# Performance work log

Hardware: AMD Instinct MI355X
Metric: run time of the kernel (lower is better)

## Reference

```python
import jax, jax.numpy as jnp
import numpy as np

B, H, W = 8, 256, 256
NF = 64          # num_feat
E = 12           # num_expert
D = NF * 4       # token dim = 256
CD = D * E       # expanded dim = 3072


def _lrelu(x):
    return jnp.where(x >= 0, x, 0.2 * x)


def _conv(x, w, stride, pad):
    return jax.lax.conv_general_dilated(
        x, w, (stride, stride), [(pad, pad), (pad, pad)],
        dimension_numbers=('NCHW', 'OIHW', 'NCHW'))


def _bn(x, g, b):
    # training-mode BatchNorm2d: batch statistics over (N, H, W)
    m = jnp.mean(x, axis=(0, 2, 3), keepdims=True)
    v = jnp.var(x, axis=(0, 2, 3), keepdims=True)
    xn = (x - m) * jax.lax.rsqrt(v + 1e-5)
    return xn * g[None, :, None, None] + b[None, :, None, None]


def setup_inputs() -> dict:
    key = jax.random.key(0)
    ks = jax.random.split(key, 16)
    s = 0.05
    d = {}
    d['x'] = jax.random.normal(ks[0], (B, 3, H, W), jnp.float32)
    d['conv0_w'] = jax.random.normal(ks[1], (NF, 3, 3, 3)) * s
    d['conv0_b'] = jnp.zeros((NF,))
    d['conv1_w'] = jax.random.normal(ks[2], (NF, NF, 4, 4)) * s
    d['bn1_g'] = jnp.ones((NF,)); d['bn1_b'] = jnp.zeros((NF,))
    d['conv2_w'] = jax.random.normal(ks[3], (2 * NF, NF, 3, 3)) * s
    d['bn2_g'] = jnp.ones((2 * NF,)); d['bn2_b'] = jnp.zeros((2 * NF,))
    d['conv3_w'] = jax.random.normal(ks[4], (2 * NF, 2 * NF, 4, 4)) * s
    d['bn3_g'] = jnp.ones((2 * NF,)); d['bn3_b'] = jnp.zeros((2 * NF,))
    d['conv4_w'] = jax.random.normal(ks[5], (4 * NF, 2 * NF, 3, 3)) * s
    d['bn4_g'] = jnp.ones((4 * NF,)); d['bn4_b'] = jnp.zeros((4 * NF,))
    d['conv5_w'] = jax.random.normal(ks[6], (4 * NF, 4 * NF, 3, 3)) * s
    d['bn5_g'] = jnp.ones((4 * NF,)); d['bn5_b'] = jnp.zeros((4 * NF,))
    d['conv6_w'] = jax.random.normal(ks[7], (4 * NF, 4 * NF, 3, 3)) * s
    d['bn6_g'] = jnp.ones((4 * NF,)); d['bn6_b'] = jnp.zeros((4 * NF,))
    d['w_gating'] = jax.random.normal(ks[8], (D, E))          # torch.randn init
    d['body_w'] = jax.random.normal(ks[9], (D, CD)) * s       # Linear(c_dim, c_dim*blocks)
    d['body_b'] = jnp.zeros((CD,))
    d['ortho_w'] = jax.random.normal(ks[10], (1, 1, CD))      # OrthorTransform weight
    d['cls_w1'] = jax.random.normal(ks[11], (D, NF // 2)) * s # shared classifier
    d['cls_b1'] = jnp.zeros((NF // 2,))
    d['cls_w2'] = jax.random.normal(ks[12], (NF // 2, 1)) * s
    d['cls_b2'] = jnp.zeros((1,))
    return d


def reference(x, conv0_w, conv0_b, conv1_w, bn1_g, bn1_b, conv2_w, bn2_g, bn2_b,
              conv3_w, bn3_g, bn3_b, conv4_w, bn4_g, bn4_b, conv5_w, bn5_g, bn5_b,
              conv6_w, bn6_g, bn6_b, w_gating, body_w, body_b, ortho_w,
              cls_w1, cls_b1, cls_w2, cls_b2):
    # --- FE conv stack ---
    h = _lrelu(_conv(x, conv0_w, 1, 1) + conv0_b[None, :, None, None])
    h = _lrelu(_bn(_conv(h, conv1_w, 2, 1), bn1_g, bn1_b))
    h = _lrelu(_bn(_conv(h, conv2_w, 1, 1), bn2_g, bn2_b))
    h = _lrelu(_bn(_conv(h, conv3_w, 2, 1), bn3_g, bn3_b))
    h = _lrelu(_bn(_conv(h, conv4_w, 1, 1), bn4_g, bn4_b))
    h = _lrelu(_bn(_conv(h, conv5_w, 1, 1), bn5_g, bn5_b))
    h = _lrelu(_bn(_conv(h, conv6_w, 1, 1), bn6_g, bn6_b))
    b, c, hh, ww = h.shape
    tok = h.reshape(b, c, hh * ww).transpose(0, 2, 1)            # (B, N, D)
    # --- softmax router ---
    routing = jax.nn.softmax(jnp.einsum('bnd,de->bne', tok, w_gating), axis=-1)
    # --- CodeReduction: Linear + lrelu, OrthorTransform multiply, lrelu ---
    feat = _lrelu(tok @ body_w + body_b)                         # (B, N, E*D)
    feat = _lrelu(feat * ortho_w)
    feat = feat.reshape(b, hh * ww, E, D)                        # torch.split chunks
    # --- shared expert MLP on every chunk (all classifiers alias one module) ---
    hid = _lrelu(jnp.einsum('bned,df->bnef', feat, cls_w1) + cls_b1)
    outs = (jnp.einsum('bnef,fo->bneo', hid, cls_w2) + cls_b2)[..., 0]  # (B,N,E)
    # --- top-1 select (equivalent to the torch.where cascade) ---
    idx = jnp.argmax(routing, axis=-1, keepdims=True)
    output = jnp.take_along_axis(outs, idx, axis=-1)             # (B, N, 1)
    return output
```

## Files before the change

kernel.cpp:

```cpp
#include <hip/hip_runtime.h>

__device__ __forceinline__ float lrelu(float x) { return x >= 0.f ? x : 0.2f * x; }

typedef const __attribute__((address_space(1))) void* gas_ptr;
typedef __attribute__((address_space(3))) void* las_ptr;

__global__ __launch_bounds__(256) void conv0_k(const float* __restrict__ x,
                                               const float* __restrict__ w,
                                               const float* __restrict__ bias,
                                               float* __restrict__ out) {
    __shared__ float sIn[3][34][34];
    __shared__ float sW[27][16];
    const int H = 256;
    int tid = threadIdx.x, tx = tid & 31, ty = tid >> 5;
    int tX = (blockIdx.x & 7) * 32, tY = (blockIdx.x >> 3) * 32;
    int b = blockIdx.y, cog = blockIdx.z * 16;
    float acc[4][16] = {};
    const float* inB = x + (size_t)b * 3 * H * H;
    for (int idx = tid; idx < 3 * 1156; idx += 256) {
        int ci = idx / 1156, r = idx % 1156, iy = r / 34, ix = r % 34;
        int gy = tY - 1 + iy, gx = tX - 1 + ix;
        float v = 0.f;
        if ((unsigned)gy < 256u && (unsigned)gx < 256u)
            v = inB[(ci * H + gy) * H + gx];
        sIn[ci][iy][ix] = v;
    }
    for (int idx = tid; idx < 27 * 16; idx += 256) {
        int co = idx & 15, rest = idx >> 4;
        sW[rest][co] = w[(cog + co) * 27 + rest];
    }
    __syncthreads();
#pragma unroll
    for (int ci = 0; ci < 3; ci++)
#pragma unroll
        for (int dy = 0; dy < 3; dy++)
#pragma unroll
            for (int dx = 0; dx < 3; dx++) {
                float a0 = sIn[ci][ty + dy][tx + dx];
                float a1 = sIn[ci][ty + 8 + dy][tx + dx];
                float a2 = sIn[ci][ty + 16 + dy][tx + dx];
                float a3 = sIn[ci][ty + 24 + dy][tx + dx];
                const float* wp = sW[ci * 9 + dy * 3 + dx];
#pragma unroll
                for (int co = 0; co < 16; co++) {
                    float wv = wp[co];
                    acc[0][co] += a0 * wv; acc[1][co] += a1 * wv;
                    acc[2][co] += a2 * wv; acc[3][co] += a3 * wv;
                }
            }
    float* outB = out + (size_t)(b * 64 + cog) * 67080;
#pragma unroll
    for (int co = 0; co < 16; co++) {
        float bv = bias[cog + co];
#pragma unroll
        for (int r = 0; r < 4; r++)
            outB[(size_t)co * 67080 + (size_t)(tY + ty + 8 * r + 1) * 260 +
                 tX + tx + 1] = lrelu(acc[r][co] + bv);
    }
}

template <int COG>
__global__ __launch_bounds__(256) void c4x4p_k(const float* __restrict__ in,
                                               const float* __restrict__ w,
                                               float* __restrict__ out,
                                               int Cin, int Cout, int Hin,
                                               int Hp, int Wp,
                                               int oHp, int oWp, int oOff) {
    __shared__ float sIn[2][4488];
    __shared__ float sW[2][16 * COG];
    const int Hout = Hin >> 1;
    const int tid = threadIdx.x, tx = tid & 31, ty = tid >> 5;
    const int tpr = Hout >> 5;
    const int tX = (blockIdx.x % tpr) * 32, tY = (blockIdx.x / tpr) * 32;
    const int b = blockIdx.y, cog = blockIdx.z * COG;
    const int HWin = Hp * Wp;
    const float* inB = in + (size_t)b * Cin * HWin;
    const int wvbase = tid & ~63;

    int gOff[5]; int lOff[5]; bool act[5];
#pragma unroll
    for (int r = 0; r < 5; r++) {
        int idx = tid + r * 256;
        bool a = idx < 1122;
        int row = idx / 17, c4 = idx % 17;
        gOff[r] = a ? ((2 * tY + row) * Wp + 2 * tX + 4 * c4) : 0;
        lOff[r] = (r * 256 + wvbase) * 4;
        act[r] = a;
    }
    const int wco = tid % COG, wt = tid / COG;
    const int wgo = ((cog + wco) * Cin) * 16 + wt;
    const bool wact = tid < 16 * COG;

    float acc[4][COG];
#pragma unroll
    for (int j = 0; j < 4; j++)
#pragma unroll
        for (int c = 0; c < COG; c++) acc[j][c] = 0.f;

#pragma unroll
    for (int r = 0; r < 5; r++)
        if (act[r])
            __builtin_amdgcn_global_load_lds((gas_ptr)(inB + gOff[r]),
                                             (las_ptr)(&sIn[0][lOff[r]]), 16, 0, 0);
    if (wact)
        __builtin_amdgcn_global_load_lds((gas_ptr)(w + wgo),
                                         (las_ptr)(&sW[0][wvbase]), 4, 0, 0);
    __syncthreads();

    for (int k = 0; k < Cin; k++) {
        const int cur = k & 1, nb = cur ^ 1;
        const bool more = (k + 1) < Cin;
        if (more) {
            const float* p = inB + (size_t)(k + 1) * HWin;
#pragma unroll
            for (int r = 0; r < 5; r++)
                if (act[r])
                    __builtin_amdgcn_global_load_lds(
                        (gas_ptr)(p + gOff[r]),
                        (las_ptr)(&sIn[nb][lOff[r]]), 16, 0, 0);
            if (wact)
                __builtin_amdgcn_global_load_lds(
                    (gas_ptr)(w + wgo + (k + 1) * 16),
                    (las_ptr)(&sW[nb][wvbase]), 4, 0, 0);
        }
        const float* sI = sIn[cur];
        const float* sw = sW[cur];
#pragma unroll
        for (int dy = 0; dy < 4; dy++)
#pragma unroll
            for (int dx = 0; dx < 4; dx++) {
                const float* bp = sI + (2 * ty + dy) * 68 + 2 * tx + dx;
                float a0 = bp[0];
                float a1 = bp[16 * 68];
                float a2 = bp[32 * 68];
                float a3 = bp[48 * 68];
                const float* wp = sw + (dy * 4 + dx) * COG;
#pragma unroll
                for (int c = 0; c < COG; c++) {
                    float wv = wp[c];
                    acc[0][c] += a0 * wv; acc[1][c] += a1 * wv;
                    acc[2][c] += a2 * wv; acc[3][c] += a3 * wv;
                }
            }
        __syncthreads();
    }

    float* outB = out + (size_t)(b * Cout + cog) * oHp * oWp;
#pragma unroll
    for (int c = 0; c < COG; c++)
#pragma unroll
        for (int r = 0; r < 4; r++)
            outB[(size_t)c * oHp * oWp +
                 (size_t)(tY + ty + 8 * r + oOff) * oWp + tX + tx + oOff] =
                acc[r][c];
}

template <int COG, bool PADDED>
__global__ __launch_bounds__(256) void c3x3_k(const float* __restrict__ in,
                                              const float* __restrict__ w,
                                              const float2* __restrict__ ss,
                                              float* __restrict__ out,
                                              int Cin, int Cout, int H,
                                              int Hp, int Wp,
                                              int oHp, int oWp, int oOff) {
    constexpr int RS = PADDED ? 36 : 34;
    constexpr int CI = 34 * RS;
    __shared__ float sIn[2][2 * CI];
    __shared__ float sW[2][18 * COG];
    const int tid = threadIdx.x, tx = tid & 31, ty = tid >> 5;
    const int tpr = H >> 5;
    const int tX = (blockIdx.x % tpr) * 32, tY = (blockIdx.x / tpr) * 32;
    const int b = blockIdx.y, cog = blockIdx.z * COG;
    const int HWin = Hp * Wp;
    const float* inB = in + (size_t)b * Cin * HWin;
    const int wvbase = tid & ~63;

    constexpr int NSTG = PADDED ? 3 : 10;
    int gOff[NSTG]; int lOff[NSTG]; float fm[NSTG]; int cis[NSTG]; bool act[NSTG];
#pragma unroll
    for (int r = 0; r < NSTG; r++) {
        int idx = tid + r * 256;
        if (PADDED) {
            bool a = idx < 612;
            int ci = idx / 306, rem = idx % 306;
            int row = rem / 9, c4 = rem % 9;
            gOff[r] = a ? (ci * HWin + (tY + row) * Wp + tX + 4 * c4) : 0;
            lOff[r] = (r * 256 + wvbase) * 4;
            act[r] = a; fm[r] = 1.f; cis[r] = ci;
        } else {
            int ci = idx / 1156, rem = idx % 1156;
            int iy = rem / 34, ix = rem % 34;
            int gy = tY - 1 + iy, gx = tX - 1 + ix;
            bool ok = (idx < 2312) && ((unsigned)gy < (unsigned)H) &&
                      ((unsigned)gx < (unsigned)H);
            gOff[r] = ok ? (ci * HWin + gy * Wp + gx) : 0;
            lOff[r] = idx;
            fm[r] = ok ? 1.f : 0.f;
            cis[r] = ci; act[r] = idx < 2312;
        }
    }
    constexpr int NW = (18 * COG + 255) / 256;
    int wgo[NW]; bool wact[NW];
#pragma unroll
    for (int r = 0; r < NW; r++) {
        int widx = tid + r * 256;
        bool a = widx < 18 * COG;
        int co = widx % COG, rest = widx / COG;
        int ci = rest / 9, t = rest % 9;
        wgo[r] = a ? (((cog + co) * Cin + ci) * 9 + t) : 0;
        wact[r] = a;
    }

    float acc[4][COG];
#pragma unroll
    for (int j = 0; j < 4; j++)
#pragma unroll
        for (int c = 0; c < COG; c++) acc[j][c] = 0.f;

    const int steps = Cin >> 1;

    if (PADDED) {
#pragma unroll
        for (int r = 0; r < NSTG; r++)
            if (act[r])
                __builtin_amdgcn_global_load_lds(
                    (gas_ptr)(inB + gOff[r]),
                    (las_ptr)(&sIn[0][lOff[r]]), 16, 0, 0);
#pragma unroll
        for (int r = 0; r < NW; r++)
            if (wact[r])
                __builtin_amdgcn_global_load_lds(
                    (gas_ptr)(w + wgo[r]),
                    (las_ptr)(&sW[0][r * 256 + wvbase]), 4, 0, 0);
    } else {
        float pw[NW];
#pragma unroll
        for (int r = 0; r < NW; r++) pw[r] = w[wgo[r]];
        float pf[NSTG];
#pragma unroll
        for (int r = 0; r < NSTG; r++) pf[r] = inB[gOff[r]];
#pragma unroll
        for (int r = 0; r < NSTG; r++)
            if (act[r]) {
                float2 t = ss[cis[r]];
                float v = t.x * pf[r] + t.y;
                sIn[0][lOff[r]] = (v >= 0.f ? v : 0.2f * v) * fm[r];
            }
#pragma unroll
        for (int r = 0; r < NW; r++)
            if (wact[r]) sW[0][tid + r * 256] = pw[r];
    }
    __syncthreads();

    for (int k = 0; k < steps; k++) {
        const int cur = k & 1;
        const int nb = cur ^ 1;
        const bool more = (k + 1) < steps;
        float pfs[PADDED ? 1 : NSTG];
        float pw[NW]; float2 t0, t1;
        if (more) {
            const int c0n = 2 * (k + 1);
            const float* p = inB + (size_t)c0n * HWin;
            const float* wp2 = w + (size_t)c0n * 9;
            if (PADDED) {
#pragma unroll
                for (int r = 0; r < NSTG; r++)
                    if (act[r])
                        __builtin_amdgcn_global_load_lds(
                            (gas_ptr)(p + gOff[r]),
                            (las_ptr)(&sIn[nb][lOff[r]]), 16, 0, 0);
#pragma unroll
                for (int r = 0; r < NW; r++)
                    if (wact[r])
                        __builtin_amdgcn_global_load_lds(
                            (gas_ptr)(wp2 + wgo[r]),
                            (las_ptr)(&sW[nb][r * 256 + wvbase]), 4, 0, 0);
            } else {
                t0 = ss[c0n]; t1 = ss[c0n + 1];
#pragma unroll
                for (int r = 0; r < NW; r++) pw[r] = wp2[wgo[r]];
#pragma unroll
                for (int r = 0; r < NSTG; r++) pfs[r] = p[gOff[r]];
            }
        }
        const float* sI = sIn[cur];
        const float* sw = sW[cur];
#pragma unroll
        for (int ci = 0; ci < 2; ci++)
#pragma unroll
            for (int dx = 0; dx < 3; dx++) {
                const float* bp = sI + ci * CI + (4 * ty) * RS + tx + dx;
                float a[6];
#pragma unroll
                for (int j = 0; j < 6; j++) a[j] = bp[j * RS];
#pragma unroll
                for (int dy = 0; dy < 3; dy++) {
                    const float* wp = sw + (ci * 9 + dy * 3 + dx) * COG;
#pragma unroll
                    for (int c = 0; c < COG; c++) {
                        float wv = wp[c];
                        acc[0][c] += a[0 + dy] * wv;
                        acc[1][c] += a[1 + dy] * wv;
                        acc[2][c] += a[2 + dy] * wv;
                        acc[3][c] += a[3 + dy] * wv;
                    }
                }
            }
        if (more && !PADDED) {
#pragma unroll
            for (int r = 0; r < NSTG; r++)
                if (act[r]) {
                    float2 t = cis[r] ? t1 : t0;
                    float v = t.x * pfs[r] + t.y;
                    sIn[nb][lOff[r]] = (v >= 0.f ? v : 0.2f * v) * fm[r];
                }
#pragma unroll
            for (int r = 0; r < NW; r++)
                if (wact[r]) sW[nb][tid + r * 256] = pw[r];
        }
        __syncthreads();
    }

    float* outB = out + (size_t)(b * Cout + cog) * oHp * oWp;
#pragma unroll
    for (int c = 0; c < COG; c++)
#pragma unroll
        for (int j = 0; j < 4; j++)
            outB[(size_t)c * oHp * oWp +
                 (size_t)(tY + 4 * ty + j + oOff) * oWp + tX + tx + oOff] =
                acc[j][c];
}

__global__ __launch_bounds__(256) void stats_k(const float* __restrict__ x,
                                               double2* __restrict__ part,
                                               int C, int hs, int ws,
                                               int Hp, int Wp, int off) {
    int c = blockIdx.y, s = blockIdx.x, S = gridDim.x;
    int H = 1 << hs, W = 1 << ws;
    int total = 8 << (hs + ws);
    int per = total / S;
    int lo = s * per;
    double sum = 0.0, sq = 0.0;
    for (int i = lo + threadIdx.x; i < lo + per; i += 256) {
        int b = i >> (hs + ws);
        int y = (i >> ws) & (H - 1);
        int xx = i & (W - 1);
        double v = x[((size_t)(b * C + c) * Hp + y + off) * Wp + xx + off];
        sum += v; sq += v * v;
    }
    __shared__ double s1[256], s2[256];
    s1[threadIdx.x] = sum; s2[threadIdx.x] = sq;
    __syncthreads();
    for (int o = 128; o; o >>= 1) {
        if (threadIdx.x < o) {
            s1[threadIdx.x] += s1[threadIdx.x + o];
            s2[threadIdx.x] += s2[threadIdx.x + o];
        }
        __syncthreads();
    }
    if (threadIdx.x == 0) { part[c * S + s].x = s1[0]; part[c * S + s].y = s2[0]; }
}

__global__ void bnfin_k(const double2* __restrict__ part, int S, int C, double invN,
                        const float* __restrict__ g, const float* __restrict__ bb,
                        float2* __restrict__ ss) {
    int c = threadIdx.x;
    if (c >= C) return;
    double sum = 0.0, sq = 0.0;
    for (int s = 0; s < S; s++) { double2 p = part[c * S + s]; sum += p.x; sq += p.y; }
    double m = sum * invN;
    double v = sq * invN - m * m;
    double sc = (double)g[c] / sqrt(v + 1e-5);
    ss[c] = make_float2((float)sc, (float)((double)bb[c] - m * sc));
}

__global__ __launch_bounds__(256) void bnact_k(float* __restrict__ p,
                                               const float2* __restrict__ ss,
                                               int C, int H, int W,
                                               int Hp, int Wp) {
    int pc = blockIdx.x;
    int c = pc & (C - 1);
    float2 t = ss ? ss[c] : make_float2(1.f, 0.f);
    bool xf = (ss != nullptr);
    float* pl = p + (size_t)pc * Hp * Wp;
    int n = Hp * Wp;
    for (int i = threadIdx.x; i < n; i += 256) {
        int y = i / Wp, x = i - y * Wp;
        bool inter = (y >= 1) && (y <= H) && (x >= 1) && (x <= W);
        if (!inter) pl[i] = 0.f;
        else if (xf) { float v = pl[i]; pl[i] = lrelu(t.x * v + t.y); }
    }
}

__global__ __launch_bounds__(256) void transp_k(const float* __restrict__ h6,
                                                const float2* __restrict__ ss,
                                                float* __restrict__ tok) {
    __shared__ float sT[32][33];
    int tx = threadIdx.x & 31, ty = threadIdx.x >> 5;
    int n0 = blockIdx.x * 32, d0 = blockIdx.y * 32, b = blockIdx.z;
    const float* hb = h6 + ((size_t)b * 256 + d0) * 4096 + n0;
#pragma unroll
    for (int r = 0; r < 4; r++) {
        int d = ty + 8 * r;
        float2 t = ss[d0 + d];
        sT[d][tx] = lrelu(t.x * hb[d * 4096 + tx] + t.y);
    }
    __syncthreads();
    float* tb = tok + ((size_t)b * 4096 + n0) * 256 + d0;
#pragma unroll
    for (int r = 0; r < 4; r++) {
        int n = ty + 8 * r;
        tb[n * 256 + tx] = sT[tx][n];
    }
}

__global__ __launch_bounds__(256) void token_k(const float* __restrict__ tok,
                                               const float* __restrict__ wg,
                                               const float* __restrict__ bw,
                                               const float* __restrict__ bb,
                                               const float* __restrict__ ow,
                                               const float* __restrict__ w1,
                                               const float* __restrict__ b1,
                                               const float* __restrict__ w2,
                                               const float* __restrict__ b2,
                                               float* __restrict__ outp) {
    __shared__ float sf[4][256];
    const int tid = threadIdx.x, wave = tid >> 6, l = tid & 63;
    const int t = blockIdx.x * 4 + wave;
    const float4 tv = reinterpret_cast<const float4*>(tok + (size_t)t * 256)[l];
    sf[wave][4 * l + 0] = tv.x; sf[wave][4 * l + 1] = tv.y;
    sf[wave][4 * l + 2] = tv.z; sf[wave][4 * l + 3] = tv.w;

    float lg[12];
#pragma unroll
    for (int e = 0; e < 12; e++) lg[e] = 0.f;
    const float tj[4] = {tv.x, tv.y, tv.z, tv.w};
#pragma unroll
    for (int j = 0; j < 4; j++) {
        const float* wr = wg + (4 * l + j) * 12;
#pragma unroll
        for (int e = 0; e < 12; e++) lg[e] += tj[j] * wr[e];
    }
#pragma unroll
    for (int off = 32; off > 0; off >>= 1) {
#pragma unroll
        for (int e = 0; e < 12; e++) lg[e] += __shfl_xor(lg[e], off);
    }
    int idx = 0; float best = lg[0];
#pragma unroll
    for (int e = 1; e < 12; e++)
        if (lg[e] > best) { best = lg[e]; idx = e; }
    const int cb = idx * 256;

    float f0 = 0.f, f1 = 0.f, f2 = 0.f, f3 = 0.f;
    const float* bwp = bw + cb + 4 * l;
#pragma unroll 4
    for (int d = 0; d < 256; d++) {
        const float td = sf[wave][d];
        const float4 wv = *reinterpret_cast<const float4*>(bwp + (size_t)d * 3072);
        f0 += td * wv.x; f1 += td * wv.y;
        f2 += td * wv.z; f3 += td * wv.w;
    }
    float fj[4] = {f0, f1, f2, f3};
#pragma unroll
    for (int j = 0; j < 4; j++) {
        int jj = cb + 4 * l + j;
        float v = lrelu(fj[j] + bb[jj]);
        v = lrelu(v * ow[jj]);
        sf[wave][4 * l + j] = v;
    }

    float o = 0.f;
    if (l < 32) {
        float h = b1[l];
#pragma unroll 4
        for (int j = 0; j < 256; j++) h += sf[wave][j] * w1[j * 32 + l];
        h = lrelu(h);
        o = h * w2[l];
    }
    o += __shfl_xor(o, 16); o += __shfl_xor(o, 8); o += __shfl_xor(o, 4);
    o += __shfl_xor(o, 2);  o += __shfl_xor(o, 1);
    if (l == 0) outp[t] = o + b2[0];
}

extern "C" void kernel_launch(void* const* d_in, const int* in_sizes, int n_in,
                              void* d_out, int out_size, void* d_ws, size_t ws_size,
                              hipStream_t stream) {
    const float* x   = (const float*)d_in[0];
    const float* w0  = (const float*)d_in[1];
    const float* b0  = (const float*)d_in[2];
    const float* w1  = (const float*)d_in[3];
    const float* g1  = (const float*)d_in[4];
    const float* be1 = (const float*)d_in[5];
    const float* w2  = (const float*)d_in[6];
    const float* g2  = (const float*)d_in[7];
    const float* be2 = (const float*)d_in[8];
    const float* w3  = (const float*)d_in[9];
    const float* g3  = (const float*)d_in[10];
    const float* be3 = (const float*)d_in[11];
    const float* w4  = (const float*)d_in[12];
    const float* g4  = (const float*)d_in[13];
    const float* be4 = (const float*)d_in[14];
    const float* w5  = (const float*)d_in[15];
    const float* g5  = (const float*)d_in[16];
    const float* be5 = (const float*)d_in[17];
    const float* w6  = (const float*)d_in[18];
    const float* g6  = (const float*)d_in[19];
    const float* be6 = (const float*)d_in[20];
    const float* wg  = (const float*)d_in[21];
    const float* bw  = (const float*)d_in[22];
    const float* bbp = (const float*)d_in[23];
    const float* owp = (const float*)d_in[24];
    const float* cw1 = (const float*)d_in[25];
    const float* cb1 = (const float*)d_in[26];
    const float* cw2 = (const float*)d_in[27];
    const float* cb2 = (const float*)d_in[28];

    char* W = (char*)d_ws;
    float2* ssb = (float2*)W;
    float2* ss1 = ssb;
    float2* ss2 = ssb + 64;
    float2* ss3 = ssb + 192;
    float2* ss4 = ssb + 320;
    float2* ss5 = ssb + 576;
    float2* ss6 = ssb + 832;
    double2* part = (double2*)(W + 16384);

    char* BIG = W + 147456;
    float* h0p = (float*)(BIG);
    float* h1  = (float*)(BIG + 70287360);
    float* h2p = (float*)(BIG);
    float* h3p = (float*)(BIG + 70287360);
    float* h4p = (float*)(BIG);
    float* h5p = (float*)(BIG + 36765696);
    float* h6  = (float*)(BIG);
    float* tok = (float*)(BIG + 36765696);

    bnact_k<<<256, 256, 0, stream>>>(h0p, nullptr, 64, 256, 256, 258, 260);
    for (int half = 0; half < 2; half++) {
        conv0_k<<<dim3(64, 4, 4), 256, 0, stream>>>(
            x + (size_t)half * 4 * 3 * 65536, w0, b0, h0p);
        c4x4p_k<8><<<dim3(16, 4, 8), 256, 0, stream>>>(
            h0p, w1, h1 + (size_t)half * 4 * 64 * 16384,
            64, 64, 256, 258, 260, 128, 128, 0);
    }
    stats_k<<<dim3(32, 64), 256, 0, stream>>>(h1, part, 64, 7, 7, 128, 128, 0);
    bnfin_k<<<1, 256, 0, stream>>>(part, 32, 64, 1.0 / 131072.0, g1, be1, ss1);
    c3x3_k<8, false><<<dim3(16, 8, 16), 256, 0, stream>>>(
        h1, w2, ss1, h2p, 64, 128, 128, 128, 128, 130, 132, 1);
    stats_k<<<dim3(32, 128), 256, 0, stream>>>(h2p, part, 128, 7, 7, 130, 132, 1);
    bnfin_k<<<1, 256, 0, stream>>>(part, 32, 128, 1.0 / 131072.0, g2, be2, ss2);
    bnact_k<<<1024, 256, 0, stream>>>(h2p, ss2, 128, 128, 128, 130, 132);
    c4x4p_k<8><<<dim3(4, 8, 16), 256, 0, stream>>>(
        h2p, w3, h3p, 128, 128, 128, 130, 132, 66, 68, 1);
    stats_k<<<dim3(32, 128), 256, 0, stream>>>(h3p, part, 128, 6, 6, 66, 68, 1);
    bnfin_k<<<1, 256, 0, stream>>>(part, 32, 128, 1.0 / 32768.0, g3, be3, ss3);
    bnact_k<<<1024, 256, 0, stream>>>(h3p, ss3, 128, 64, 64, 66, 68);
    c3x3_k<8, true><<<dim3(4, 8, 32), 256, 0, stream>>>(
        h3p, w4, nullptr, h4p, 128, 256, 64, 66, 68, 66, 68, 1);
    stats_k<<<dim3(32, 256), 256, 0, stream>>>(h4p, part, 256, 6, 6, 66, 68, 1);
    bnfin_k<<<1, 256, 0, stream>>>(part, 32, 256, 1.0 / 32768.0, g4, be4, ss4);
    bnact_k<<<2048, 256, 0, stream>>>(h4p, ss4, 256, 64, 64, 66, 68);
    c3x3_k<8, true><<<dim3(4, 8, 32), 256, 0, stream>>>(
        h4p, w5, nullptr, h5p, 256, 256, 64, 66, 68, 66, 68, 1);
    stats_k<<<dim3(32, 256), 256, 0, stream>>>(h5p, part, 256, 6, 6, 66, 68, 1);
    bnfin_k<<<1, 256, 0, stream>>>(part, 32, 256, 1.0 / 32768.0, g5, be5, ss5);
    bnact_k<<<2048, 256, 0, stream>>>(h5p, ss5, 256, 64, 64, 66, 68);
    c3x3_k<8, true><<<dim3(4, 8, 32), 256, 0, stream>>>(
        h5p, w6, nullptr, h6, 256, 256, 64, 66, 68, 64, 64, 0);
    stats_k<<<dim3(32, 256), 256, 0, stream>>>(h6, part, 256, 6, 6, 64, 64, 0);
    bnfin_k<<<1, 256, 0, stream>>>(part, 32, 256, 1.0 / 32768.0, g6, be6, ss6);
    transp_k<<<dim3(128, 8, 8), 256, 0, stream>>>(h6, ss6, tok);
    token_k<<<8192, 256, 0, stream>>>(tok, wg, bw, bbp, owp, cw1, cb1, cw2, cb2,
                                      (float*)d_out);
}
```

Measured before the change: 2.799 ms.

## Fuse BatchNorm statistics into conv epilogues and unify 3x3 conv on padded path

```diff
diff --git a/kernel.cpp b/kernel.cpp
--- a/kernel.cpp
+++ b/kernel.cpp
@@ -60,9 +60,43 @@
 }
 
 template <int COG>
+__device__ __forceinline__ void stats_epilogue(float (&acc)[4][COG], float* red,
+                                               double2* part, int cog,
+                                               int slotBase, int S, int tid) {
+#pragma unroll
+    for (int c = 0; c < COG; c++) {
+        float s = 0.f, q = 0.f;
+#pragma unroll
+        for (int j = 0; j < 4; j++) { float v = acc[j][c]; s += v; q += v * v; }
+        red[c * 256 + tid] = s;
+        red[COG * 256 + c * 256 + tid] = q;
+    }
+    __syncthreads();
+    for (int off = 128; off; off >>= 1) {
+        if (tid < off) {
+#pragma unroll
+            for (int c = 0; c < COG; c++) {
+                red[c * 256 + tid] += red[c * 256 + tid + off];
+                red[COG * 256 + c * 256 + tid] +=
+                    red[COG * 256 + c * 256 + tid + off];
+            }
+        }
+        __syncthreads();
+    }
+    if (tid < COG) {
+        int slot = slotBase + blockIdx.y * gridDim.x + blockIdx.x;
+        part[(size_t)(cog + tid) * S + slot].x = (double)red[tid * 256];
+        part[(size_t)(cog + tid) * S + slot].y =
+            (double)red[COG * 256 + tid * 256];
+    }
+}
+
+template <int COG>
 __global__ __launch_bounds__(256) void c4x4p_k(const float* __restrict__ in,
                                                const float* __restrict__ w,
                                                float* __restrict__ out,
+                                               double2* __restrict__ part,
+                                               int slotBase, int S,
                                                int Cin, int Cout, int Hin,
                                                int Hp, int Wp,
                                                int oHp, int oWp, int oOff) {
@@ -153,17 +187,19 @@
             outB[(size_t)c * oHp * oWp +
                  (size_t)(tY + ty + 8 * r + oOff) * oWp + tX + tx + oOff] =
                 acc[r][c];
-}
-
-template <int COG, bool PADDED>
+    stats_epilogue<COG>(acc, &sIn[0][0], part, cog, slotBase, S, tid);
+}
+
+template <int COG>
 __global__ __launch_bounds__(256) void c3x3_k(const float* __restrict__ in,
                                               const float* __restrict__ w,
-                                              const float2* __restrict__ ss,
                                               float* __restrict__ out,
+                                              double2* __restrict__ part,
+                                              int slotBase, int S,
                                               int Cin, int Cout, int H,
                                               int Hp, int Wp,
                                               int oHp, int oWp, int oOff) {
-    constexpr int RS = PADDED ? 36 : 34;
+    constexpr int RS = 36;
     constexpr int CI = 34 * RS;
     __shared__ float sIn[2][2 * CI];
     __shared__ float sW[2][18 * COG];
@@ -175,29 +211,16 @@
     const float* inB = in + (size_t)b * Cin * HWin;
     const int wvbase = tid & ~63;
 
-    constexpr int NSTG = PADDED ? 3 : 10;
-    int gOff[NSTG]; int lOff[NSTG]; float fm[NSTG]; int cis[NSTG]; bool act[NSTG];
-#pragma unroll
-    for (int r = 0; r < NSTG; r++) {
+    int gOff[3]; int lOff[3]; bool act[3];
+#pragma unroll
+    for (int r = 0; r < 3; r++) {
         int idx = tid + r * 256;
-        if (PADDED) {
-            bool a = idx < 612;
-            int ci = idx / 306, rem = idx % 306;
-            int row = rem / 9, c4 = rem % 9;
-            gOff[r] = a ? (ci * HWin + (tY + row) * Wp + tX + 4 * c4) : 0;
-            lOff[r] = (r * 256 + wvbase) * 4;
-            act[r] = a; fm[r] = 1.f; cis[r] = ci;
-        } else {
-            int ci = idx / 1156, rem = idx % 1156;
-            int iy = rem / 34, ix = rem % 34;
-            int gy = tY - 1 + iy, gx = tX - 1 + ix;
-            bool ok = (idx < 2312) && ((unsigned)gy < (unsigned)H) &&
-                      ((unsigned)gx < (unsigned)H);
-            gOff[r] = ok ? (ci * HWin + gy * Wp + gx) : 0;
-            lOff[r] = idx;
-            fm[r] = ok ? 1.f : 0.f;
-            cis[r] = ci; act[r] = idx < 2312;
-        }
+        bool a = idx < 612;
+        int ci = idx / 306, rem = idx % 306;
+        int row = rem / 9, c4 = rem % 9;
+        gOff[r] = a ? (ci * HWin + (tY + row) * Wp + tX + 4 * c4) : 0;
+        lOff[r] = (r * 256 + wvbase) * 4;
+        act[r] = a;
     }
     constexpr int NW = (18 * COG + 255) / 256;
     int wgo[NW]; bool wact[NW];
@@ -219,69 +242,40 @@
 
     const int steps = Cin >> 1;
 
-    if (PADDED) {
-#pragma unroll
-        for (int r = 0; r < NSTG; r++)
-            if (act[r])
-                __builtin_amdgcn_global_load_lds(
-                    (gas_ptr)(inB + gOff[r]),
-                    (las_ptr)(&sIn[0][lOff[r]]), 16, 0, 0);
-#pragma unroll
-        for (int r = 0; r < NW; r++)
-            if (wact[r])
-                __builtin_amdgcn_global_load_lds(
-                    (gas_ptr)(w + wgo[r]),
-                    (las_ptr)(&sW[0][r * 256 + wvbase]), 4, 0, 0);
-    } else {
-        float pw[NW];
-#pragma unroll
-        for (int r = 0; r < NW; r++) pw[r] = w[wgo[r]];
-        float pf[NSTG];
-#pragma unroll
-        for (int r = 0; r < NSTG; r++) pf[r] = inB[gOff[r]];
-#pragma unroll
-        for (int r = 0; r < NSTG; r++)
-            if (act[r]) {
-                float2 t = ss[cis[r]];
-                float v = t.x * pf[r] + t.y;
-                sIn[0][lOff[r]] = (v >= 0.f ? v : 0.2f * v) * fm[r];
-            }
-#pragma unroll
-        for (int r = 0; r < NW; r++)
-            if (wact[r]) sW[0][tid + r * 256] = pw[r];
-    }
+#pragma unroll
+    for (int r = 0; r < 3; r++)
+        if (act[r])
+            __builtin_amdgcn_global_load_lds(
+                (gas_ptr)(inB + gOff[r]),
+                (las_ptr)(&sIn[0][lOff[r]]), 16, 0, 0);
+#pragma unroll
+    for (int r = 0; r < NW; r++)
+        if (wact[r])
+            __builtin_amdgcn_global_load_lds(
+                (gas_ptr)(w + wgo[r]),
+                (las_ptr)(&sW[0][r * 256 + wvbase]), 4, 0, 0);
     __syncthreads();
 
     for (int k = 0; k < steps; k++) {
         const int cur = k & 1;
         const int nb = cur ^ 1;
         const bool more = (k + 1) < steps;
-        float pfs[PADDED ? 1 : NSTG];
-        float pw[NW]; float2 t0, t1;
         if (more) {
             const int c0n = 2 * (k + 1);
             const float* p = inB + (size_t)c0n * HWin;
             const float* wp2 = w + (size_t)c0n * 9;
-            if (PADDED) {
-#pragma unroll
-                for (int r = 0; r < NSTG; r++)
-                    if (act[r])
-                        __builtin_amdgcn_global_load_lds(
-                            (gas_ptr)(p + gOff[r]),
-                            (las_ptr)(&sIn[nb][lOff[r]]), 16, 0, 0);
-#pragma unroll
-                for (int r = 0; r < NW; r++)
-                    if (wact[r])
-                        __builtin_amdgcn_global_load_lds(
-                            (gas_ptr)(wp2 + wgo[r]),
-                            (las_ptr)(&sW[nb][r * 256 + wvbase]), 4, 0, 0);
-            } else {
-                t0 = ss[c0n]; t1 = ss[c0n + 1];
-#pragma unroll
-                for (int r = 0; r < NW; r++) pw[r] = wp2[wgo[r]];
-#pragma unroll
-                for (int r = 0; r < NSTG; r++) pfs[r] = p[gOff[r]];
-            }
+#pragma unroll
+            for (int r = 0; r < 3; r++)
+                if (act[r])
+                    __builtin_amdgcn_global_load_lds(
+                        (gas_ptr)(p + gOff[r]),
+                        (las_ptr)(&sIn[nb][lOff[r]]), 16, 0, 0);
+#pragma unroll
+            for (int r = 0; r < NW; r++)
+                if (wact[r])
+                    __builtin_amdgcn_global_load_lds(
+                        (gas_ptr)(wp2 + wgo[r]),
+                        (las_ptr)(&sW[nb][r * 256 + wvbase]), 4, 0, 0);
         }
         const float* sI = sIn[cur];
         const float* sw = sW[cur];
@@ -306,18 +300,6 @@
                     }
                 }
             }
-        if (more && !PADDED) {
-#pragma unroll
-            for (int r = 0; r < NSTG; r++)
-                if (act[r]) {
-                    float2 t = cis[r] ? t1 : t0;
-                    float v = t.x * pfs[r] + t.y;
-                    sIn[nb][lOff[r]] = (v >= 0.f ? v : 0.2f * v) * fm[r];
-                }
-#pragma unroll
-            for (int r = 0; r < NW; r++)
-                if (wact[r]) sW[nb][tid + r * 256] = pw[r];
-        }
         __syncthreads();
     }
 
@@ -329,36 +311,7 @@
             outB[(size_t)c * oHp * oWp +
                  (size_t)(tY + 4 * ty + j + oOff) * oWp + tX + tx + oOff] =
                 acc[j][c];
-}
-
-__global__ __launch_bounds__(256) void stats_k(const float* __restrict__ x,
-                                               double2* __restrict__ part,
-                                               int C, int hs, int ws,
-                                               int Hp, int Wp, int off) {
-    int c = blockIdx.y, s = blockIdx.x, S = gridDim.x;
-    int H = 1 << hs, W = 1 << ws;
-    int total = 8 << (hs + ws);
-    int per = total / S;
-    int lo = s * per;
-    double sum = 0.0, sq = 0.0;
-    for (int i = lo + threadIdx.x; i < lo + per; i += 256) {
-        int b = i >> (hs + ws);
-        int y = (i >> ws) & (H - 1);
-        int xx = i & (W - 1);
-        double v = x[((size_t)(b * C + c) * Hp + y + off) * Wp + xx + off];
-        sum += v; sq += v * v;
-    }
-    __shared__ double s1[256], s2[256];
-    s1[threadIdx.x] = sum; s2[threadIdx.x] = sq;
-    __syncthreads();
-    for (int o = 128; o; o >>= 1) {
-        if (threadIdx.x < o) {
-            s1[threadIdx.x] += s1[threadIdx.x + o];
-            s2[threadIdx.x] += s2[threadIdx.x + o];
-        }
-        __syncthreads();
-    }
-    if (threadIdx.x == 0) { part[c * S + s].x = s1[0]; part[c * S + s].y = s2[0]; }
+    stats_epilogue<COG>(acc, &sIn[0][0], part, cog, slotBase, S, tid);
 }
 
 __global__ void bnfin_k(const double2* __restrict__ part, int S, int C, double invN,
@@ -367,7 +320,10 @@
     int c = threadIdx.x;
     if (c >= C) return;
     double sum = 0.0, sq = 0.0;
-    for (int s = 0; s < S; s++) { double2 p = part[c * S + s]; sum += p.x; sq += p.y; }
+    for (int s = 0; s < S; s++) {
+        double2 p = part[(size_t)c * S + s];
+        sum += p.x; sq += p.y;
+    }
     double m = sum * invN;
     double v = sq * invN - m * m;
     double sc = (double)g[c] / sqrt(v + 1e-5);
@@ -526,9 +482,9 @@
     float2* ss6 = ssb + 832;
     double2* part = (double2*)(W + 16384);
 
-    char* BIG = W + 147456;
+    char* BIG = W + 278528;
     float* h0p = (float*)(BIG);
-    float* h1  = (float*)(BIG + 70287360);
+    float* h1p = (float*)(BIG + 70287360);
     float* h2p = (float*)(BIG);
     float* h3p = (float*)(BIG + 70287360);
     float* h4p = (float*)(BIG);
@@ -541,34 +497,29 @@
         conv0_k<<<dim3(64, 4, 4), 256, 0, stream>>>(
             x + (size_t)half * 4 * 3 * 65536, w0, b0, h0p);
         c4x4p_k<8><<<dim3(16, 4, 8), 256, 0, stream>>>(
-            h0p, w1, h1 + (size_t)half * 4 * 64 * 16384,
-            64, 64, 256, 258, 260, 128, 128, 0);
-    }
-    stats_k<<<dim3(32, 64), 256, 0, stream>>>(h1, part, 64, 7, 7, 128, 128, 0);
-    bnfin_k<<<1, 256, 0, stream>>>(part, 32, 64, 1.0 / 131072.0, g1, be1, ss1);
-    c3x3_k<8, false><<<dim3(16, 8, 16), 256, 0, stream>>>(
-        h1, w2, ss1, h2p, 64, 128, 128, 128, 128, 130, 132, 1);
-    stats_k<<<dim3(32, 128), 256, 0, stream>>>(h2p, part, 128, 7, 7, 130, 132, 1);
-    bnfin_k<<<1, 256, 0, stream>>>(part, 32, 128, 1.0 / 131072.0, g2, be2, ss2);
+            h0p, w1, h1p + (size_t)half * 4 * 64 * 17160, part, half * 64, 128,
+            64, 64, 256, 258, 260, 130, 132, 1);
+    }
+    bnfin_k<<<1, 256, 0, stream>>>(part, 128, 64, 1.0 / 131072.0, g1, be1, ss1);
+    bnact_k<<<512, 256, 0, stream>>>(h1p, ss1, 64, 128, 128, 130, 132);
+    c3x3_k<8><<<dim3(16, 8, 16), 256, 0, stream>>>(
+        h1p, w2, h2p, part, 0, 128, 64, 128, 128, 130, 132, 130, 132, 1);
+    bnfin_k<<<1, 256, 0, stream>>>(part, 128, 128, 1.0 / 131072.0, g2, be2, ss2);
     bnact_k<<<1024, 256, 0, stream>>>(h2p, ss2, 128, 128, 128, 130, 132);
     c4x4p_k<8><<<dim3(4, 8, 16), 256, 0, stream>>>(
-        h2p, w3, h3p, 128, 128, 128, 130, 132, 66, 68, 1);
-    stats_k<<<dim3(32, 128), 256, 0, stream>>>(h3p, part, 128, 6, 6, 66, 68, 1);
+        h2p, w3, h3p, part, 0, 32, 128, 128, 128, 130, 132, 66, 68, 1);
     bnfin_k<<<1, 256, 0, stream>>>(part, 32, 128, 1.0 / 32768.0, g3, be3, ss3);
     bnact_k<<<1024, 256, 0, stream>>>(h3p, ss3, 128, 64, 64, 66, 68);
-    c3x3_k<8, true><<<dim3(4, 8, 32), 256, 0, stream>>>(
-        h3p, w4, nullptr, h4p, 128, 256, 64, 66, 68, 66, 68, 1);
-    stats_k<<<dim3(32, 256), 256, 0, stream>>>(h4p, part, 256, 6, 6, 66, 68, 1);
+    c3x3_k<8><<<dim3(4, 8, 32), 256, 0, stream>>>(
+        h3p, w4, h4p, part, 0, 32, 128, 256, 64, 66, 68, 66, 68, 1);
     bnfin_k<<<1, 256, 0, stream>>>(part, 32, 256, 1.0 / 32768.0, g4, be4, ss4);
     bnact_k<<<2048, 256, 0, stream>>>(h4p, ss4, 256, 64, 64, 66, 68);
-    c3x3_k<8, true><<<dim3(4, 8, 32), 256, 0, stream>>>(
-        h4p, w5, nullptr, h5p, 256, 256, 64, 66, 68, 66, 68, 1);
-    stats_k<<<dim3(32, 256), 256, 0, stream>>>(h5p, part, 256, 6, 6, 66, 68, 1);
+    c3x3_k<8><<<dim3(4, 8, 32), 256, 0, stream>>>(
+        h4p, w5, h5p, part, 0, 32, 256, 256, 64, 66, 68, 66, 68, 1);
     bnfin_k<<<1, 256, 0, stream>>>(part, 32, 256, 1.0 / 32768.0, g5, be5, ss5);
     bnact_k<<<2048, 256, 0, stream>>>(h5p, ss5, 256, 64, 64, 66, 68);
-    c3x3_k<8, true><<<dim3(4, 8, 32), 256, 0, stream>>>(
-        h5p, w6, nullptr, h6, 256, 256, 64, 66, 68, 64, 64, 0);
-    stats_k<<<dim3(32, 256), 256, 0, stream>>>(h6, part, 256, 6, 6, 64, 64, 0);
+    c3x3_k<8><<<dim3(4, 8, 32), 256, 0, stream>>>(
+        h5p, w6, h6, part, 0, 32, 256, 256, 64, 66, 68, 64, 64, 0);
     bnfin_k<<<1, 256, 0, stream>>>(part, 32, 256, 1.0 / 32768.0, g6, be6, ss6);
     transp_k<<<dim3(128, 8, 8), 256, 0, stream>>>(h6, ss6, tok);
     token_k<<<8192, 256, 0, stream>>>(tok, wg, bw, bbp, owp, cw1, cb1, cw2, cb2,
```

After: 2.583 ms. 7.7% less time.
